# Optimization experiments

Hardware: AMD Instinct MI355X
Metric: run time of the kernel (lower is better)

The kernel has to match this reference:

```python
import jax, jax.numpy as jnp
import numpy as np

TAU = 2.0          # LIF membrane time constant (tau=2.0 in module)
SG_ALPHA = 4.0     # spikingjelly default Sigmoid surrogate alpha


def lif(x, v_th=1.0):
    """MultiStepLIFNode: leaky-integrate-fire over leading time dim T.
    v <- v + (x - v)/tau ; spike = H(v - v_th) ; hard reset v <- 0 where spiked.
    Surrogate gradient (sigmoid) via straight-through for backward.
    x: [T, ...] -> spikes: [T, ...]
    """
    def step(v, xt):
        v = v + (xt - v) / TAU
        sg = jax.nn.sigmoid(SG_ALPHA * (v - v_th))
        hard = (v >= v_th).astype(xt.dtype)
        spike = jax.lax.stop_gradient(hard - sg) + sg
        # detach_reset=True: reset path does not carry gradient
        v = v * (1.0 - jax.lax.stop_gradient(spike))
        return v, spike
    v0 = jnp.zeros_like(x[0])
    _, s = jax.lax.scan(step, v0, x)
    return s


def bn_c(x, scale, bias):
    """Inference-mode BatchNorm folded to per-channel affine; x: [T,B,C,N]."""
    return x * scale[None, None, :, None] + bias[None, None, :, None]


def setup_inputs() -> dict:
    T, B, C, H, W = 4, 32, 512, 14, 14
    Ch = int(C * 4.0)  # mlp hidden
    key = jax.random.key(0)
    ks = jax.random.split(key, 16)
    std = 0.05
    d = {
        'x': jax.random.normal(ks[0], (T, B, C, H, W), jnp.float32),
        'q_w': jax.random.normal(ks[1], (C, C), jnp.float32) * std,
        'q_bn_s': 1.0 + 0.1 * jax.random.normal(ks[2], (C,), jnp.float32),
        'q_bn_b': 0.1 * jax.random.normal(ks[3], (C,), jnp.float32),
        'k_w': jax.random.normal(ks[4], (C, C), jnp.float32) * std,
        'k_bn_s': 1.0 + 0.1 * jax.random.normal(ks[5], (C,), jnp.float32),
        'k_bn_b': 0.1 * jax.random.normal(ks[6], (C,), jnp.float32),
        'proj_w': jax.random.normal(ks[7], (C, C), jnp.float32) * std,
        'proj_b': 0.1 * jax.random.normal(ks[8], (C,), jnp.float32),
        'proj_bn_s': 1.0 + 0.1 * jax.random.normal(ks[9], (C,), jnp.float32),
        'proj_bn_b': 0.1 * jax.random.normal(ks[10], (C,), jnp.float32),
        'mlp1_w': jax.random.normal(ks[11], (Ch, C), jnp.float32) * std,
        'mlp1_b': 0.1 * jax.random.normal(ks[12], (Ch,), jnp.float32),
        'mlp1_bn_s': 1.0 + 0.1 * jax.random.normal(ks[13], (Ch,), jnp.float32),
        'mlp1_bn_b': 0.1 * jax.random.normal(ks[14], (Ch,), jnp.float32),
        'mlp2_w': jax.random.normal(ks[15], (C, Ch), jnp.float32) * std,
        'mlp2_b': 0.1 * jax.random.normal(jax.random.fold_in(key, 100), (C,), jnp.float32),
        'mlp2_bn_s': 1.0 + 0.1 * jax.random.normal(jax.random.fold_in(key, 101), (C,), jnp.float32),
        'mlp2_bn_b': 0.1 * jax.random.normal(jax.random.fold_in(key, 102), (C,), jnp.float32),
    }
    return d


NUM_HEADS = 8


def reference(x, q_w, q_bn_s, q_bn_b, k_w, k_bn_s, k_bn_b,
              proj_w, proj_b, proj_bn_s, proj_bn_b,
              mlp1_w, mlp1_b, mlp1_bn_s, mlp1_bn_b,
              mlp2_w, mlp2_b, mlp2_bn_s, mlp2_bn_b):
    T, B, C, H, W = x.shape
    N = H * W
    h = NUM_HEADS
    Chd = C // h
    xf = x.reshape(T, B, C, N)

    # ---- Token_QK_Attention ----
    q_sp = lif(bn_c(jnp.einsum('oc,tbcn->tbon', q_w, xf), q_bn_s, q_bn_b))
    k_sp = lif(bn_c(jnp.einsum('oc,tbcn->tbon', k_w, xf), k_bn_s, k_bn_b))
    # per-head channel sum of q spikes: [T,B,h,1,N]
    q_sum = q_sp.reshape(T, B, h, Chd, N).sum(axis=3, keepdims=True)
    attn_sp = lif(q_sum, v_th=0.5)                       # attn_lif, v_threshold=0.5
    x_one = attn_sp * k_sp.reshape(T, B, h, Chd, N)      # spiking multiply
    x_one = x_one.reshape(T, B, C, N)
    p = jnp.einsum('oc,tbcn->tbon', proj_w, x_one) + proj_b[None, None, :, None]
    y = lif(bn_c(p, proj_bn_s, proj_bn_b)).reshape(T, B, C, H, W)
    x = x + y                                            # residual

    # ---- MLP ----
    xf = x.reshape(T, B, C, N)
    h1 = jnp.einsum('oc,tbcn->tbon', mlp1_w, xf) + mlp1_b[None, None, :, None]
    h1 = lif(bn_c(h1, mlp1_bn_s, mlp1_bn_b))
    h2 = jnp.einsum('oc,tbcn->tbon', mlp2_w, h1) + mlp2_b[None, None, :, None]
    h2 = lif(bn_c(h2, mlp2_bn_s, mlp2_bn_b))
    return x + h2.reshape(T, B, C, H, W)
```

## Files before the change

kernel.cpp:

```cpp
#include <hip/hip_runtime.h>
#include <cstdint>

#define NT  4
#define NB  32
#define NC  512
#define NCH 2048
#define NN  196
#define NM  (NB * NN)
#define NH  8

struct GP {
    const float *q_bn_s, *q_bn_b, *k_bn_s, *k_bn_b;
    const float *proj_b, *proj_bn_s, *proj_bn_b;
    const float *mlp1_b, *mlp1_bn_s, *mlp1_bn_b;
    const float *mlp2_b, *mlp2_bn_s, *mlp2_bn_b;
    const float *wqkT, *wprojT, *wmlp1T, *wmlp2T;
    const float *xT;
    float *xy;
    float *v_q, *v_k, *v_y, *v_h1, *v_h2, *v_attn;
    unsigned char *q_sp, *k_sp, *x_one, *h1_sp, *attn_sp;
    float *out;
    int t;
};

__device__ __forceinline__ float lif_step(float z, float v_old, float vth, int& sp) {
    float d = __fsub_rn(z, v_old);
    float h = __fmul_rn(d, 0.5f);
    float v = __fadd_rn(v_old, h);
    sp = (v >= vth) ? 1 : 0;
    return sp ? 0.0f : v;
}

typedef const void __attribute__((address_space(1))) gas_t;
typedef void __attribute__((address_space(3))) las_t;
__device__ __forceinline__ void gl_lds16(const float* g, float* l) {
    __builtin_amdgcn_global_load_lds((gas_t*)g, (las_t*)l, 16, 0, 0);
}
__device__ __forceinline__ void vm0() {
    asm volatile("s_waitcnt vmcnt(0)" ::: "memory");
}
__device__ __forceinline__ void lgkm0() {
    asm volatile("s_waitcnt lgkmcnt(0)" ::: "memory");
}


__global__ __launch_bounds__(256) void trw_k(const float* __restrict__ src,
                                             float* __restrict__ dst,
                                             int K, int ldD, int offD) {
    __shared__ float tle[32][33];
    const int c0 = blockIdx.x * 32, o0 = blockIdx.y * 32;
    const int tx = threadIdx.x & 31, ty = threadIdx.x >> 5;
#pragma unroll
    for (int r = 0; r < 4; ++r)
        tle[ty + r * 8][tx] = src[(size_t)(o0 + ty + r * 8) * K + c0 + tx];
    __syncthreads();
#pragma unroll
    for (int r = 0; r < 4; ++r)
        dst[(size_t)(c0 + ty + r * 8) * ldD + offD + o0 + tx] = tle[tx][ty + r * 8];
}

__global__ __launch_bounds__(64) void permx_k(const float* __restrict__ x,
                                              float* __restrict__ xT) {
    const int id = blockIdx.x;
    const int b = id & 31;
    const int c = (id >> 5) & 511;
    const int t = id >> 14;
    const float* s = x + ((size_t)(t * NB + b) * NC + c) * NN;
    float* d = xT + ((size_t)(t * NC + c) * NB + b) * NN;
    for (int n = threadIdx.x; n < NN; n += 64) d[n] = s[n];
}

__global__ __launch_bounds__(256) void attn_k(GP gp) {
    const int m = blockIdx.x * 256 + threadIdx.x;
    const int h = blockIdx.y;
    if (m >= NM) return;
    const unsigned char* q = gp.q_sp + (size_t)h * 64 * NM + m;
    int s = 0;
#pragma unroll 8
    for (int d = 0; d < 64; ++d) s += q[(size_t)d * NM];
    float v = gp.t ? gp.v_attn[(size_t)h * NM + m] : 0.0f;
    int sp;
    v = lif_step((float)s, v, 0.5f, sp);
    gp.v_attn[(size_t)h * NM + m] = v;
    gp.attn_sp[(size_t)h * NM + m] = (unsigned char)sp;
}

__global__ __launch_bounds__(256) void xone_k(GP gp) {
    const int c = blockIdx.y;
    const int m4 = (blockIdx.x * 256 + threadIdx.x) * 4;
    if (m4 >= NM) return;
    const unsigned int kv = *(const unsigned int*)(gp.k_sp + (size_t)c * NM + m4);
    const unsigned int av = *(const unsigned int*)(gp.attn_sp + (size_t)(c >> 6) * NM + m4);
    *(unsigned int*)(gp.x_one + (size_t)c * NM + m4) = kv & av;
}

template <int MODE>
__global__ __launch_bounds__(64) void gemm_lif(GP gp) {
    constexpr bool FUSED = (MODE == 1 || MODE == 3);
    constexpr int K_TOT = (MODE == 3) ? 2048 : 512;
    constexpr int LDA = (MODE == 0) ? 1024 : (MODE == 2) ? 2048 : 512;
    constexpr int BK = 16;
    constexpr int NIT = K_TOT / BK;
    constexpr int MT = FUSED ? 32 : 64;
    constexpr int RN = FUSED ? 4 : 8;

    __shared__ float As[2][BK][32];
    __shared__ float Xs[2][BK][MT];

    const int lane = threadIdx.x;
    const int to = lane & 7;
    const int tn = lane >> 3;
    const int m0 = blockIdx.x * MT;
    const int ot = blockIdx.y;
    const int o0 = ot * 32;
    const int mb = m0 + tn * RN;

    const float* wA = (MODE == 0) ? gp.wqkT : (MODE == 1) ? gp.wprojT
                    : (MODE == 2) ? gp.wmlp1T : gp.wmlp2T;
    const float* xf = (MODE == 0) ? gp.xT + (size_t)gp.t * NC * NM : gp.xy;
    const unsigned char* xu = (MODE == 1) ? gp.x_one : gp.h1_sp;

    auto stageA = [&](int buf, int s) {
#pragma unroll
        for (int r = 0; r < 2; ++r)
            gl_lds16(wA + (size_t)(s * BK + r * 8 + (lane >> 3)) * LDA + o0 + (lane & 7) * 4,
                     &As[buf][r * 8][0]);
    };
    auto stageXf = [&](int buf, int s) {
#pragma unroll
        for (int r = 0; r < 4; ++r)
            gl_lds16(xf + (size_t)(s * BK + r * 4 + (lane >> 4)) * NM + m0 + (lane & 15) * 4,
                     &Xs[buf][r * 4][0]);
    };
    const int xrow = lane >> 2;
    const int xcb = (lane & 3) * 8;
    auto loadB = [&](int s) -> uint2 {
        return *(const uint2*)(xu + (size_t)(s * BK + xrow) * NM + m0 + xcb);
    };
    auto flushB = [&](int buf, uint2 xb) {
        float* d = &Xs[buf][xrow][xcb];
        float4 f0, f1;
        f0.x = (float)(unsigned char)(xb.x);
        f0.y = (float)(unsigned char)(xb.x >> 8);
        f0.z = (float)(unsigned char)(xb.x >> 16);
        f0.w = (float)(xb.x >> 24);
        f1.x = (float)(unsigned char)(xb.y);
        f1.y = (float)(unsigned char)(xb.y >> 8);
        f1.z = (float)(unsigned char)(xb.y >> 16);
        f1.w = (float)(xb.y >> 24);
        *(float4*)d = f0;
        *(float4*)(d + 4) = f1;
    };

    float acc[4][RN];
#pragma unroll
    for (int i = 0; i < 4; ++i)
#pragma unroll
        for (int j = 0; j < RN; ++j) acc[i][j] = 0.0f;

    auto compute = [&](int cur) {
        if constexpr (!FUSED) {
#pragma unroll 4
            for (int kk = 0; kk < BK; ++kk) {
                const float4 av = *(const float4*)&As[cur][kk][to * 4];
                const float4 x0 = *(const float4*)&Xs[cur][kk][tn * 8];
                const float4 x1 = *(const float4*)&Xs[cur][kk][tn * 8 + 4];
                const float a4[4] = {av.x, av.y, av.z, av.w};
                const float x8[8] = {x0.x, x0.y, x0.z, x0.w, x1.x, x1.y, x1.z, x1.w};
#pragma unroll
                for (int i = 0; i < 4; ++i)
#pragma unroll
                    for (int j = 0; j < 8; ++j)
                        acc[i][j] = __fadd_rn(acc[i][j], __fmul_rn(a4[i], x8[j]));
            }
        } else {
#pragma unroll 8
            for (int kk = 0; kk < BK; ++kk) {
                const float4 av = *(const float4*)&As[cur][kk][to * 4];
                const float4 xv = *(const float4*)&Xs[cur][kk][tn * 4];
                const float a4[4] = {av.x, av.y, av.z, av.w};
                const float x4[4] = {xv.x, xv.y, xv.z, xv.w};
#pragma unroll
                for (int i = 0; i < 4; ++i)
#pragma unroll
                    for (int j = 0; j < 4; ++j)
                        acc[i][j] = __fmaf_rn(a4[i], x4[j], acc[i][j]);
            }
        }
    };

    if constexpr (!FUSED) {
        stageA(0, 0); stageXf(0, 0);
        vm0();
    } else {
        stageA(0, 0);
        uint2 xb = loadB(0);
        vm0();
        flushB(0, xb);
        lgkm0();
    }

#pragma unroll 1
    for (int it = 0; it < NIT; ++it) {
        const int cur = it & 1;
        const int nxt = cur ^ 1;
        const bool more = (it + 1 < NIT);
        if constexpr (!FUSED) {
            if (more) { stageA(nxt, it + 1); stageXf(nxt, it + 1); }
            compute(cur);
            if (more) vm0();
        } else {
            uint2 xb = {0, 0};
            if (more) { stageA(nxt, it + 1); xb = loadB(it + 1); }
            compute(cur);
            if (more) { vm0(); flushB(nxt, xb); lgkm0(); }
        }
    }

    if constexpr (MODE == 0) {
        const bool isq = (ot < 16);
        const float* bs = isq ? gp.q_bn_s : gp.k_bn_s;
        const float* bbv = isq ? gp.q_bn_b : gp.k_bn_b;
        float* vb = isq ? gp.v_q : gp.v_k;
        unsigned char* sb = isq ? gp.q_sp : gp.k_sp;
        const int ob = (ot & 15) * 32;
#pragma unroll
        for (int i = 0; i < 4; ++i) {
            const int oo = ob + to * 4 + i;
            const float sc = bs[oo], bc = bbv[oo];
            float* vr = vb + (size_t)oo * NM + mb;
            float vv[8];
            if (gp.t) {
                const float4 v0 = *(const float4*)vr, v1 = *(const float4*)(vr + 4);
                vv[0] = v0.x; vv[1] = v0.y; vv[2] = v0.z; vv[3] = v0.w;
                vv[4] = v1.x; vv[5] = v1.y; vv[6] = v1.z; vv[7] = v1.w;
            } else {
#pragma unroll
                for (int j = 0; j < 8; ++j) vv[j] = 0.0f;
            }
            unsigned int pk[2] = {0, 0};
#pragma unroll
            for (int j = 0; j < 8; ++j) {
                const float z = __fadd_rn(__fmul_rn(acc[i][j], sc), bc);
                int sp;
                vv[j] = lif_step(z, vv[j], 1.0f, sp);
                pk[j >> 2] |= (unsigned)sp << ((j & 3) * 8);
            }
            *(float4*)vr = make_float4(vv[0], vv[1], vv[2], vv[3]);
            *(float4*)(vr + 4) = make_float4(vv[4], vv[5], vv[6], vv[7]);
            *(unsigned int*)(sb + (size_t)oo * NM + mb) = pk[0];
            *(unsigned int*)(sb + (size_t)oo * NM + mb + 4) = pk[1];
        }
    } else if constexpr (MODE == 2) {
        const int ob = ot * 32;
#pragma unroll
        for (int i = 0; i < 4; ++i) {
            const int o = ob + to * 4 + i;
            const float bi = gp.mlp1_b[o], sc = gp.mlp1_bn_s[o], bc = gp.mlp1_bn_b[o];
            float* vr = gp.v_h1 + (size_t)o * NM + mb;
            float vv[8];
            if (gp.t) {
                const float4 v0 = *(const float4*)vr, v1 = *(const float4*)(vr + 4);
                vv[0] = v0.x; vv[1] = v0.y; vv[2] = v0.z; vv[3] = v0.w;
                vv[4] = v1.x; vv[5] = v1.y; vv[6] = v1.z; vv[7] = v1.w;
            } else {
#pragma unroll
                for (int j = 0; j < 8; ++j) vv[j] = 0.0f;
            }
            unsigned int pk[2] = {0, 0};
#pragma unroll
            for (int j = 0; j < 8; ++j) {
                const float z = __fadd_rn(__fmul_rn(__fadd_rn(acc[i][j], bi), sc), bc);
                int sp;
                vv[j] = lif_step(z, vv[j], 1.0f, sp);
                pk[j >> 2] |= (unsigned)sp << ((j & 3) * 8);
            }
            *(float4*)vr = make_float4(vv[0], vv[1], vv[2], vv[3]);
            *(float4*)(vr + 4) = make_float4(vv[4], vv[5], vv[6], vv[7]);
            *(unsigned int*)(gp.h1_sp + (size_t)o * NM + mb) = pk[0];
            *(unsigned int*)(gp.h1_sp + (size_t)o * NM + mb + 4) = pk[1];
        }
    } else if constexpr (MODE == 1) {
        const int ob = ot * 32;
#pragma unroll
        for (int i = 0; i < 4; ++i) {
            const int o = ob + to * 4 + i;
            const float bi = gp.proj_b[o], sc = gp.proj_bn_s[o], bc = gp.proj_bn_b[o];
            float* vr = gp.v_y + (size_t)o * NM + mb;
            const float4 vld = gp.t ? *(const float4*)vr : make_float4(0, 0, 0, 0);
            const float4 xv4 = *(const float4*)(gp.xT + ((size_t)gp.t * NC + o) * NM + mb);
            float vv[4] = {vld.x, vld.y, vld.z, vld.w};
            const float xvv[4] = {xv4.x, xv4.y, xv4.z, xv4.w};
            float xyo[4];
#pragma unroll
            for (int j = 0; j < 4; ++j) {
                const float z = __fadd_rn(__fmul_rn(__fadd_rn(acc[i][j], bi), sc), bc);
                int sp;
                vv[j] = lif_step(z, vv[j], 1.0f, sp);
                xyo[j] = __fadd_rn(xvv[j], (float)sp);
            }
            *(float4*)vr = make_float4(vv[0], vv[1], vv[2], vv[3]);
            *(float4*)(gp.xy + (size_t)o * NM + mb) = make_float4(xyo[0], xyo[1], xyo[2], xyo[3]);
        }
    } else {
        const int ob = ot * 32;
        const int b = mb / NN;
        const int n = mb - b * NN;
#pragma unroll
        for (int i = 0; i < 4; ++i) {
            const int o = ob + to * 4 + i;
            const float bi = gp.mlp2_b[o], sc = gp.mlp2_bn_s[o], bc = gp.mlp2_bn_b[o];
            float* vr = gp.v_h2 + (size_t)o * NM + mb;
            const float4 vld = gp.t ? *(const float4*)vr : make_float4(0, 0, 0, 0);
            const float4 xyv = *(const float4*)(gp.xy + (size_t)o * NM + mb);
            float vv[4] = {vld.x, vld.y, vld.z, vld.w};
            const float xyf[4] = {xyv.x, xyv.y, xyv.z, xyv.w};
            float ov[4];
#pragma unroll
            for (int j = 0; j < 4; ++j) {
                const float z = __fadd_rn(__fmul_rn(__fadd_rn(acc[i][j], bi), sc), bc);
                int sp;
                vv[j] = lif_step(z, vv[j], 1.0f, sp);
                ov[j] = __fadd_rn(xyf[j], (float)sp);
            }
            *(float4*)&gp.out[(((size_t)gp.t * NB + b) * NC + o) * NN + n] =
                make_float4(ov[0], ov[1], ov[2], ov[3]);
            *(float4*)vr = make_float4(vv[0], vv[1], vv[2], vv[3]);
        }
    }
}

extern "C" void kernel_launch(void* const* d_in, const int* in_sizes, int n_in,
                              void* d_out, int out_size, void* d_ws, size_t ws_size,
                              hipStream_t stream) {
    const float* x       = (const float*)d_in[0];
    const float* q_w     = (const float*)d_in[1];
    const float* k_w     = (const float*)d_in[4];
    const float* proj_w  = (const float*)d_in[7];
    const float* mlp1_w  = (const float*)d_in[11];
    const float* mlp2_w  = (const float*)d_in[15];

    GP gp;
    gp.q_bn_s = (const float*)d_in[2];  gp.q_bn_b = (const float*)d_in[3];
    gp.k_bn_s = (const float*)d_in[5];  gp.k_bn_b = (const float*)d_in[6];
    gp.proj_b = (const float*)d_in[8];  gp.proj_bn_s = (const float*)d_in[9];  gp.proj_bn_b = (const float*)d_in[10];
    gp.mlp1_b = (const float*)d_in[12]; gp.mlp1_bn_s = (const float*)d_in[13]; gp.mlp1_bn_b = (const float*)d_in[14];
    gp.mlp2_b = (const float*)d_in[16]; gp.mlp2_bn_s = (const float*)d_in[17]; gp.mlp2_bn_b = (const float*)d_in[18];
    gp.out = (float*)d_out;

    char* ws = (char*)d_ws;
    size_t off = 0;
    auto alloc = [&](size_t bytes) -> void* {
        void* r = ws + off;
        off += (bytes + 255) & ~(size_t)255;
        return r;
    };
    float* wqkT   = (float*)alloc((size_t)512 * 1024 * 4);
    float* wprojT = (float*)alloc((size_t)512 * 512 * 4);
    float* wmlp1T = (float*)alloc((size_t)512 * 2048 * 4);
    float* wmlp2T = (float*)alloc((size_t)2048 * 512 * 4);
    float* xT     = (float*)alloc((size_t)NT * NC * NM * 4);
    gp.xy     = (float*)alloc((size_t)NC * NM * 4);
    gp.v_q    = (float*)alloc((size_t)NC * NM * 4);
    gp.v_k    = (float*)alloc((size_t)NC * NM * 4);
    gp.v_y    = (float*)alloc((size_t)NC * NM * 4);
    gp.v_h2   = (float*)alloc((size_t)NC * NM * 4);
    gp.v_h1   = (float*)alloc((size_t)NCH * NM * 4);
    gp.v_attn = (float*)alloc((size_t)NH * NM * 4);
    gp.q_sp   = (unsigned char*)alloc((size_t)NC * NM);
    gp.k_sp   = (unsigned char*)alloc((size_t)NC * NM);
    gp.x_one  = (unsigned char*)alloc((size_t)NC * NM);
    gp.h1_sp  = (unsigned char*)alloc((size_t)NCH * NM);
    gp.attn_sp= (unsigned char*)alloc((size_t)NH * NM);
    gp.wqkT = wqkT; gp.wprojT = wprojT; gp.wmlp1T = wmlp1T; gp.wmlp2T = wmlp2T;
    gp.xT = xT;

    trw_k<<<dim3(16, 16), 256, 0, stream>>>(q_w,    wqkT,   512,  1024, 0);
    trw_k<<<dim3(16, 16), 256, 0, stream>>>(k_w,    wqkT,   512,  1024, 512);
    trw_k<<<dim3(16, 16), 256, 0, stream>>>(proj_w, wprojT, 512,  512,  0);
    trw_k<<<dim3(16, 64), 256, 0, stream>>>(mlp1_w, wmlp1T, 512,  2048, 0);
    trw_k<<<dim3(64, 16), 256, 0, stream>>>(mlp2_w, wmlp2T, 2048, 512,  0);
    permx_k<<<NT * NC * NB, 64, 0, stream>>>(x, xT);

    for (int t = 0; t < NT; ++t) {
        gp.t = t;
        gemm_lif<0><<<dim3(98, 32), 64, 0, stream>>>(gp);
        attn_k<<<dim3(25, NH), 256, 0, stream>>>(gp);
        xone_k<<<dim3(7, NC), 256, 0, stream>>>(gp);
        gemm_lif<1><<<dim3(196, 16), 64, 0, stream>>>(gp);
        gemm_lif<2><<<dim3(98, 64), 64, 0, stream>>>(gp);
        gemm_lif<3><<<dim3(196, 16), 64, 0, stream>>>(gp);
    }
}
```

Baseline: 2.586 ms.

## Deepen fused GEMM pipeline to prefetch two stages ahead with four LDS buffers

For the fused GEMM modes (spike-input proj and mlp2), the kernel now uses four shared-memory buffers and issues loads two K-steps ahead. It waits with a partial vmcnt so one stage's loads stay in flight while the current tile is computed. The X tile row is also padded (36 floats) to reduce LDS bank conflicts. The cost is more LDS per block and careful counter accounting. If the vmcnt(3) count does not match the number of loads per stage, the code reads stale data.

```diff
diff --git a/kernel.cpp b/kernel.cpp
--- a/kernel.cpp
+++ b/kernel.cpp
@@ -39,6 +39,9 @@
 __device__ __forceinline__ void vm0() {
     asm volatile("s_waitcnt vmcnt(0)" ::: "memory");
 }
+__device__ __forceinline__ void vm3() {
+    asm volatile("s_waitcnt vmcnt(3)" ::: "memory");
+}
 __device__ __forceinline__ void lgkm0() {
     asm volatile("s_waitcnt lgkmcnt(0)" ::: "memory");
 }
@@ -103,9 +106,11 @@
     constexpr int NIT = K_TOT / BK;
     constexpr int MT = FUSED ? 32 : 64;
     constexpr int RN = FUSED ? 4 : 8;
-
-    __shared__ float As[2][BK][32];
-    __shared__ float Xs[2][BK][MT];
+    constexpr int NBUF = FUSED ? 4 : 2;
+    constexpr int XP = FUSED ? 36 : MT;
+
+    __shared__ float As[NBUF][BK][32];
+    __shared__ float Xs[NBUF][BK][XP];
 
     const int lane = threadIdx.x;
     const int to = lane & 7;
@@ -192,28 +197,37 @@
     if constexpr (!FUSED) {
         stageA(0, 0); stageXf(0, 0);
         vm0();
-    } else {
-        stageA(0, 0);
-        uint2 xb = loadB(0);
-        vm0();
-        flushB(0, xb);
-        lgkm0();
-    }
-
 #pragma unroll 1
-    for (int it = 0; it < NIT; ++it) {
-        const int cur = it & 1;
-        const int nxt = cur ^ 1;
-        const bool more = (it + 1 < NIT);
-        if constexpr (!FUSED) {
-            if (more) { stageA(nxt, it + 1); stageXf(nxt, it + 1); }
+        for (int it = 0; it < NIT; ++it) {
+            const int cur = it & 1;
+            const bool more = (it + 1 < NIT);
+            if (more) { stageA(cur ^ 1, it + 1); stageXf(cur ^ 1, it + 1); }
             compute(cur);
             if (more) vm0();
-        } else {
-            uint2 xb = {0, 0};
-            if (more) { stageA(nxt, it + 1); xb = loadB(it + 1); }
-            compute(cur);
-            if (more) { vm0(); flushB(nxt, xb); lgkm0(); }
+        }
+    } else {
+        uint2 sl0, sl1;
+        stageA(0, 0); sl0 = loadB(0);
+        stageA(1, 1); sl1 = loadB(1);
+        vm3();
+        flushB(0, sl0);
+        lgkm0();
+
+        auto body = [&](int i, int cb, uint2& sStage, uint2& sFlush) {
+            if (i + 2 < NIT) { stageA((cb + 2) & 3, i + 2); sStage = loadB(i + 2); }
+            compute(cb);
+            if (i + 1 < NIT) {
+                if (NIT - 1 - i >= 2) vm3(); else vm0();
+                flushB((cb + 1) & 3, sFlush);
+                lgkm0();
+            }
+        };
+#pragma unroll 1
+        for (int i = 0; i < NIT; i += 4) {
+            body(i + 0, 0, sl0, sl1);
+            body(i + 1, 1, sl1, sl0);
+            body(i + 2, 2, sl0, sl1);
+            body(i + 3, 3, sl1, sl0);
         }
     }
 
```

After: 2.517 ms. 2.7% less time.
